# Optimization experiments

Hardware: AMD Instinct MI355X
Metric: run time of the kernel (lower is better)

## Reference

```python
import jax, jax.numpy as jnp
import numpy as np

MARGIN = 1.0

def setup_inputs() -> dict:
    key = jax.random.key(0)
    k1, k2 = jax.random.split(key)
    B, C = 16384, 1000
    outputs = jax.random.normal(k1, (B, C), dtype=jnp.float32)
    labels = jax.random.normal(k2, (B, C), dtype=jnp.float32)
    return {"outputs": outputs, "labels": labels}

def reference(outputs, labels):
    # sign(labels): +1 where labels >= 0, else -1 (matches np.where(l >= 0, 1.0, -1.0))
    sign = jnp.where(labels >= 0, 1.0, -1.0).astype(outputs.dtype)
    # per-class hinge: mean over batch of clamp(margin - out * sign, min=0),
    # then summed over classes -> equivalent to sum of per-class means.
    hinge = jnp.maximum(MARGIN - outputs * sign, 0.0)  # [B, C]
    loss = jnp.sum(jnp.mean(hinge, axis=0))            # sum over classes of batch-mean
    return loss
```

## Files before the change

kernel.cpp:

```cpp
#include <hip/hip_runtime.h>


constexpr int BLOCK  = 256;
constexpr int UNROLL = 8;
constexpr int TILE   = BLOCK * UNROLL;

__device__ __forceinline__ float block_reduce(float acc, float* wave_sums) {
    #pragma unroll
    for (int off = 32; off > 0; off >>= 1)
        acc += __shfl_down(acc, off, 64);
    const int lane = threadIdx.x & 63;
    const int wid  = threadIdx.x >> 6;
    if (lane == 0) wave_sums[wid] = acc;
    __syncthreads();
    float s = 0.0f;
    #pragma unroll
    for (int w = 0; w < BLOCK / 64; ++w) s += wave_sums[w];
    return s;
}

__global__ __launch_bounds__(BLOCK) void hinge_stage1_exact(
    const float4* __restrict__ out4,
    const float4* __restrict__ lab4,
    float* __restrict__ partials)
{
    const int tid = threadIdx.x;
    const size_t base = (size_t)blockIdx.x * TILE + tid;
    const float4* __restrict__ po = out4 + base;
    const float4* __restrict__ pl = lab4 + base;

    float4 o[UNROLL], l[UNROLL];
    #pragma unroll
    for (int u = 0; u < UNROLL; ++u) o[u] = po[u * BLOCK];
    #pragma unroll
    for (int u = 0; u < UNROLL; ++u) l[u] = pl[u * BLOCK];

    float a0 = 0.f, a1 = 0.f, a2 = 0.f, a3 = 0.f;
    #pragma unroll
    for (int u = 0; u < UNROLL; ++u) {
        a0 += fmaxf(1.0f - (l[u].x >= 0.0f ? o[u].x : -o[u].x), 0.0f);
        a1 += fmaxf(1.0f - (l[u].y >= 0.0f ? o[u].y : -o[u].y), 0.0f);
        a2 += fmaxf(1.0f - (l[u].z >= 0.0f ? o[u].z : -o[u].z), 0.0f);
        a3 += fmaxf(1.0f - (l[u].w >= 0.0f ? o[u].w : -o[u].w), 0.0f);
    }
    float acc = (a0 + a1) + (a2 + a3);

    __shared__ float wave_sums[BLOCK / 64];
    const float s = block_reduce(acc, wave_sums);
    if (tid == 0) partials[blockIdx.x] = s;
}

__global__ __launch_bounds__(BLOCK) void hinge_stage1_guarded(
    const float4* __restrict__ out4,
    const float4* __restrict__ lab4,
    float* __restrict__ partials,
    int n4)
{
    const int tid = threadIdx.x;
    const long long base = (long long)blockIdx.x * TILE + tid;
    float acc = 0.0f;
    #pragma unroll
    for (int u = 0; u < UNROLL; ++u) {
        const long long idx = base + (long long)u * BLOCK;
        if (idx < n4) {
            const float4 o = out4[idx];
            const float4 l = lab4[idx];
            acc += fmaxf(1.0f - (l.x >= 0.0f ? o.x : -o.x), 0.0f);
            acc += fmaxf(1.0f - (l.y >= 0.0f ? o.y : -o.y), 0.0f);
            acc += fmaxf(1.0f - (l.z >= 0.0f ? o.z : -o.z), 0.0f);
            acc += fmaxf(1.0f - (l.w >= 0.0f ? o.w : -o.w), 0.0f);
        }
    }
    __shared__ float wave_sums[BLOCK / 64];
    const float s = block_reduce(acc, wave_sums);
    if (tid == 0) partials[blockIdx.x] = s;
}

__global__ __launch_bounds__(BLOCK) void hinge_stage2_kernel(
    const float* __restrict__ partials,
    float* __restrict__ loss,
    int n_partials, float inv_b)
{
    float acc = 0.0f;
    for (int i = threadIdx.x; i < n_partials; i += BLOCK)
        acc += partials[i];
    __shared__ float wave_sums[BLOCK / 64];
    const float s = block_reduce(acc, wave_sums);
    if (threadIdx.x == 0) loss[0] = s * inv_b;
}

extern "C" void kernel_launch(void* const* d_in, const int* in_sizes, int n_in,
                              void* d_out, int out_size, void* d_ws, size_t ws_size,
                              hipStream_t stream) {
    const float* outputs = (const float*)d_in[0];
    const float* labels  = (const float*)d_in[1];
    float* loss     = (float*)d_out;
    float* partials = (float*)d_ws;

    const long long n = (long long)in_sizes[0];
    const int n4 = (int)(n / 4);
    const float inv_b = 1.0f / 16384.0f;

    const int grid = (n4 + TILE - 1) / TILE;

    if (n4 % TILE == 0) {
        hinge_stage1_exact<<<grid, BLOCK, 0, stream>>>(
            (const float4*)outputs, (const float4*)labels, partials);
    } else {
        hinge_stage1_guarded<<<grid, BLOCK, 0, stream>>>(
            (const float4*)outputs, (const float4*)labels, partials, n4);
    }
    hinge_stage2_kernel<<<1, BLOCK, 0, stream>>>(partials, loss, grid, inv_b);
}
```

Baseline: 27.34 us.

## Fuse final reduction into main kernel with atomic ticket and enlarge tiles

Replaces the two-kernel reduction with a single kernel on the exact-tile path. Each block writes its partial sum, then takes a ticket with an atomic counter, and the last block to arrive reduces all partials and resets the counter. This removes the second launch and its dependency gap. Tiles also grow to 512 threads × 16 float4s, which cuts the grid to 500 blocks and interleaves loads inside the loop instead of prefetching them all up front. The risks are lower memory-level parallelism per CU and reliance on the workspace ticket starting at zero, or at a multiple of the grid size.

```diff
diff --git a/kernel.cpp b/kernel.cpp
--- a/kernel.cpp
+++ b/kernel.cpp
@@ -1,9 +1,10 @@
 #include <hip/hip_runtime.h>
 
 
-constexpr int BLOCK  = 256;
-constexpr int UNROLL = 8;
+constexpr int BLOCK  = 512;
+constexpr int UNROLL = 16;
 constexpr int TILE   = BLOCK * UNROLL;
+constexpr int NWAVES = BLOCK / 64;
 
 __device__ __forceinline__ float block_reduce(float acc, float* wave_sums) {
     #pragma unroll
@@ -15,53 +16,71 @@
     __syncthreads();
     float s = 0.0f;
     #pragma unroll
-    for (int w = 0; w < BLOCK / 64; ++w) s += wave_sums[w];
+    for (int w = 0; w < NWAVES; ++w) s += wave_sums[w];
     return s;
 }
 
-__global__ __launch_bounds__(BLOCK) void hinge_stage1_exact(
+__global__ __launch_bounds__(BLOCK) void hinge_fused_ticket(
     const float4* __restrict__ out4,
     const float4* __restrict__ lab4,
-    float* __restrict__ partials)
+    float* __restrict__ partials,
+    unsigned* __restrict__ ticket,
+    float* __restrict__ loss,
+    int grid_n, float inv_b)
 {
     const int tid = threadIdx.x;
     const size_t base = (size_t)blockIdx.x * TILE + tid;
     const float4* __restrict__ po = out4 + base;
     const float4* __restrict__ pl = lab4 + base;
 
-    float4 o[UNROLL], l[UNROLL];
-    #pragma unroll
-    for (int u = 0; u < UNROLL; ++u) o[u] = po[u * BLOCK];
-    #pragma unroll
-    for (int u = 0; u < UNROLL; ++u) l[u] = pl[u * BLOCK];
-
     float a0 = 0.f, a1 = 0.f, a2 = 0.f, a3 = 0.f;
     #pragma unroll
     for (int u = 0; u < UNROLL; ++u) {
-        a0 += fmaxf(1.0f - (l[u].x >= 0.0f ? o[u].x : -o[u].x), 0.0f);
-        a1 += fmaxf(1.0f - (l[u].y >= 0.0f ? o[u].y : -o[u].y), 0.0f);
-        a2 += fmaxf(1.0f - (l[u].z >= 0.0f ? o[u].z : -o[u].z), 0.0f);
-        a3 += fmaxf(1.0f - (l[u].w >= 0.0f ? o[u].w : -o[u].w), 0.0f);
+        const float4 o = po[u * BLOCK];
+        const float4 l = pl[u * BLOCK];
+        a0 += fmaxf(1.0f - (l.x >= 0.0f ? o.x : -o.x), 0.0f);
+        a1 += fmaxf(1.0f - (l.y >= 0.0f ? o.y : -o.y), 0.0f);
+        a2 += fmaxf(1.0f - (l.z >= 0.0f ? o.z : -o.z), 0.0f);
+        a3 += fmaxf(1.0f - (l.w >= 0.0f ? o.w : -o.w), 0.0f);
     }
     float acc = (a0 + a1) + (a2 + a3);
 
-    __shared__ float wave_sums[BLOCK / 64];
+    __shared__ float wave_sums[NWAVES];
+    __shared__ unsigned is_last;
     const float s = block_reduce(acc, wave_sums);
-    if (tid == 0) partials[blockIdx.x] = s;
+
+    if (tid == 0) {
+        partials[blockIdx.x] = s;
+        __threadfence();
+        const unsigned t = atomicAdd(ticket, 1u);
+        is_last = ((t % (unsigned)grid_n) == (unsigned)(grid_n - 1)) ? 1u : 0u;
+    }
+    __syncthreads();
+
+    if (is_last) {
+        __threadfence();
+        float a = (tid < grid_n) ? partials[tid] : 0.0f;
+        __syncthreads();
+        const float t2 = block_reduce(a, wave_sums);
+        if (tid == 0) {
+            loss[0] = t2 * inv_b;
+            atomicExch(ticket, 0u);
+        }
+    }
 }
 
-__global__ __launch_bounds__(BLOCK) void hinge_stage1_guarded(
+__global__ __launch_bounds__(256) void hinge_stage1_guarded(
     const float4* __restrict__ out4,
     const float4* __restrict__ lab4,
     float* __restrict__ partials,
     int n4)
 {
     const int tid = threadIdx.x;
-    const long long base = (long long)blockIdx.x * TILE + tid;
+    const long long base = (long long)blockIdx.x * (256LL * 8) + tid;
     float acc = 0.0f;
     #pragma unroll
-    for (int u = 0; u < UNROLL; ++u) {
-        const long long idx = base + (long long)u * BLOCK;
+    for (int u = 0; u < 8; ++u) {
+        const long long idx = base + (long long)u * 256;
         if (idx < n4) {
             const float4 o = out4[idx];
             const float4 l = lab4[idx];
@@ -71,22 +90,30 @@
             acc += fmaxf(1.0f - (l.w >= 0.0f ? o.w : -o.w), 0.0f);
         }
     }
-    __shared__ float wave_sums[BLOCK / 64];
-    const float s = block_reduce(acc, wave_sums);
-    if (tid == 0) partials[blockIdx.x] = s;
+    #pragma unroll
+    for (int off = 32; off > 0; off >>= 1)
+        acc += __shfl_down(acc, off, 64);
+    __shared__ float ws[4];
+    if ((tid & 63) == 0) ws[tid >> 6] = acc;
+    __syncthreads();
+    if (tid == 0) partials[blockIdx.x] = ws[0] + ws[1] + ws[2] + ws[3];
 }
 
-__global__ __launch_bounds__(BLOCK) void hinge_stage2_kernel(
+__global__ __launch_bounds__(256) void hinge_stage2_kernel(
     const float* __restrict__ partials,
     float* __restrict__ loss,
     int n_partials, float inv_b)
 {
     float acc = 0.0f;
-    for (int i = threadIdx.x; i < n_partials; i += BLOCK)
+    for (int i = threadIdx.x; i < n_partials; i += 256)
         acc += partials[i];
-    __shared__ float wave_sums[BLOCK / 64];
-    const float s = block_reduce(acc, wave_sums);
-    if (threadIdx.x == 0) loss[0] = s * inv_b;
+    #pragma unroll
+    for (int off = 32; off > 0; off >>= 1)
+        acc += __shfl_down(acc, off, 64);
+    __shared__ float ws[4];
+    if ((threadIdx.x & 63) == 0) ws[threadIdx.x >> 6] = acc;
+    __syncthreads();
+    if (threadIdx.x == 0) loss[0] = (ws[0] + ws[1] + ws[2] + ws[3]) * inv_b;
 }
 
 extern "C" void kernel_launch(void* const* d_in, const int* in_sizes, int n_in,
@@ -94,21 +121,24 @@
                               hipStream_t stream) {
     const float* outputs = (const float*)d_in[0];
     const float* labels  = (const float*)d_in[1];
-    float* loss     = (float*)d_out;
-    float* partials = (float*)d_ws;
+    float* loss = (float*)d_out;
+
+    unsigned* ticket  = (unsigned*)d_ws;
+    float* partials   = (float*)((char*)d_ws + 256);
 
     const long long n = (long long)in_sizes[0];
     const int n4 = (int)(n / 4);
     const float inv_b = 1.0f / 16384.0f;
 
-    const int grid = (n4 + TILE - 1) / TILE;
-
     if (n4 % TILE == 0) {
-        hinge_stage1_exact<<<grid, BLOCK, 0, stream>>>(
-            (const float4*)outputs, (const float4*)labels, partials);
+        const int grid = n4 / TILE;
+        hinge_fused_ticket<<<grid, BLOCK, 0, stream>>>(
+            (const float4*)outputs, (const float4*)labels,
+            partials, ticket, loss, grid, inv_b);
     } else {
-        hinge_stage1_guarded<<<grid, BLOCK, 0, stream>>>(
+        const int grid = (n4 + 256 * 8 - 1) / (256 * 8);
+        hinge_stage1_guarded<<<grid, 256, 0, stream>>>(
             (const float4*)outputs, (const float4*)labels, partials, n4);
+        hinge_stage2_kernel<<<1, 256, 0, stream>>>(partials, loss, grid, inv_b);
     }
-    hinge_stage2_kernel<<<1, BLOCK, 0, stream>>>(partials, loss, grid, inv_b);
 }
```

After: 39.45 us. +44.3%, slower.
